# Performance work log

Measured on AMD Instinct MI355X. Metric: run time of the kernel, lower is better.

The kernel has to match this reference:

```python
import jax, jax.numpy as jnp
import numpy as np

N_NODES = 100000
N_EDGES = 600000
N_GRAPHS = 512
VOCAB = 4096
EMB = 128
HID = 128


def setup_inputs() -> dict:
    key = jax.random.key(0)
    ks = jax.random.split(key, 8)
    x = jax.random.randint(ks[0], (N_NODES,), 0, VOCAB)
    edge_index = jax.random.randint(ks[1], (2, N_EDGES), 0, N_NODES)
    batch = jnp.sort(jax.random.randint(ks[2], (N_NODES,), 0, N_GRAPHS))
    emb = jax.random.normal(ks[3], (VOCAB, EMB), dtype=jnp.float32)
    W1 = jax.random.normal(ks[4], (EMB, HID), dtype=jnp.float32) / np.sqrt(EMB)
    b1 = jnp.zeros((HID,), dtype=jnp.float32)
    W2 = jax.random.normal(ks[5], (HID, HID), dtype=jnp.float32) / np.sqrt(HID)
    b2 = jnp.zeros((HID,), dtype=jnp.float32)
    return {"x": x, "edge_index": edge_index, "batch": batch,
            "emb": emb, "W1": W1, "b1": b1, "W2": W2, "b2": b2}


def gcn_conv(h, src, dst, W, b, n_nodes):
    # PyG GCNConv: linear transform, then symmetric-normalized scatter-sum
    # (self-loops already included in src/dst), plus bias.
    h = h @ W
    deg = jax.ops.segment_sum(jnp.ones(dst.shape, h.dtype), dst, num_segments=n_nodes)
    dis = jnp.where(deg > 0, jax.lax.rsqrt(jnp.maximum(deg, 1.0)), 0.0)
    norm = dis[src] * dis[dst]                      # [E]
    msg = h[src] * norm[:, None]                    # gather + scale
    out = jax.ops.segment_sum(msg, dst, num_segments=n_nodes)
    return out + b


def reference(x, edge_index, batch, emb, W1, b1, W2, b2):
    n = x.shape[0]
    loop = jnp.arange(n)
    src = jnp.concatenate([edge_index[0], loop])    # add self-loops, as GCNConv does
    dst = jnp.concatenate([edge_index[1], loop])

    h = emb[x]                                      # [N, EMB] embedding lookup
    h = jax.nn.relu(gcn_conv(h, src, dst, W1, b1, n))
    # dropout: identity in eval mode
    h = gcn_conv(h, src, dst, W2, b2, n)            # [N, HID]

    # global_mean_pool over graph ids
    sums = jax.ops.segment_sum(h, batch, num_segments=N_GRAPHS)
    cnts = jax.ops.segment_sum(jnp.ones((n,), h.dtype), batch, num_segments=N_GRAPHS)
    return sums / jnp.maximum(cnts, 1.0)[:, None]   # [N_GRAPHS, HID]
```

## Files before the change

### kernel.cpp

```cpp
#include <hip/hip_runtime.h>
#include <hip/hip_bf16.h>
#include <hip/hip_fp16.h>

#define D 128

__device__ __forceinline__ float bf2f(unsigned short u) {
  return __uint_as_float(((unsigned int)u) << 16);
}
__device__ __forceinline__ unsigned short f2bf(float f) {
  unsigned int x = __float_as_uint(f);
  x += 0x7fff + ((x >> 16) & 1);
  return (unsigned short)(x >> 16);
}
__device__ __forceinline__ float h2f(unsigned short b) {
  return __half2float(__ushort_as_half(b));
}


__global__ void k_prep(const unsigned short* __restrict__ t0, int n0,
                       const unsigned short* __restrict__ t1, int n1,
                       const unsigned short* __restrict__ t2, int n2,
                       const unsigned short* __restrict__ t3, int n3,
                       const unsigned short* __restrict__ t4, int n4,
                       const unsigned int* __restrict__ ei32,
                       int* __restrict__ flag, int* __restrict__ indeg,
                       float* __restrict__ P, int nn, int ngD) {
  int b = blockIdx.x;
  if (b < 5) {
    const unsigned short* tabs[5] = {t0, t1, t2, t3, t4};
    int ns[5] = {n0, n1, n2, n3, n4};
    const unsigned short* u16 = tabs[b];
    int n = ns[b];
    __shared__ int cnt;
    int K = n / 2 < 256 ? n / 2 : 256;
    if (threadIdx.x == 0) cnt = 0;
    __syncthreads();
    if (threadIdx.x < K) {
      unsigned short u = u16[threadIdx.x * 2];
      int e = (u >> 7) & 0xFF;
      if (u == 0 || (e >= 100 && e <= 140)) atomicAdd(&cnt, 1);
    }
    __syncthreads();
    if (threadIdx.x == 0) flag[b] = (cnt * 2 >= K) ? 1 : 0;
  } else if (b == 5) {
    __shared__ int z;
    if (threadIdx.x == 0) z = 0;
    __syncthreads();
    if (threadIdx.x < 64 && ei32[threadIdx.x * 2 + 1] == 0u) atomicAdd(&z, 1);
    __syncthreads();
    if (threadIdx.x == 0) flag[5] = (z >= 60) ? 1 : 0;
  } else {
    int i = (b - 6) * 256 + threadIdx.x;
    if (i < nn) indeg[i] = 0;
    int j = i - nn;
    if (j >= 0 && j < ngD) P[j] = 0.f;
  }
}

__global__ void k_convi_all(const void* __restrict__ xr, const void* __restrict__ eir,
                            const void* __restrict__ br,
                            int* __restrict__ xs, int* __restrict__ srcs,
                            int* __restrict__ dsts, int* __restrict__ batchs,
                            int* __restrict__ indeg,
                            int nn, int ne, int vocab, int ng,
                            const int* __restrict__ flag64) {
  long long i = (long long)blockIdx.x * blockDim.x + threadIdx.x;
  int is64 = *flag64;
  if (i < nn) {
    int v = is64 ? (int)((const long long*)xr)[i] : ((const int*)xr)[i];
    v = v < 0 ? 0 : (v > vocab - 1 ? vocab - 1 : v);
    xs[i] = v;
  } else if (i < (long long)nn + ne) {
    long long j = i - nn;
    int v = is64 ? (int)((const long long*)eir)[j] : ((const int*)eir)[j];
    v = v < 0 ? 0 : (v > nn - 1 ? nn - 1 : v);
    srcs[j] = v;
  } else if (i < (long long)nn + 2 * ne) {
    long long j = i - nn - ne;
    int v = is64 ? (int)((const long long*)eir)[ne + j] : ((const int*)eir)[ne + j];
    v = v < 0 ? 0 : (v > nn - 1 ? nn - 1 : v);
    dsts[j] = v;
    atomicAdd(&indeg[v], 1);
  } else if (i < 2LL * nn + 2 * ne) {
    long long j = i - nn - 2 * ne;
    int v = is64 ? (int)((const long long*)br)[j] : ((const int*)br)[j];
    v = v < 0 ? 0 : (v > ng - 1 ? ng - 1 : v);
    batchs[j] = v;
  }
}

__global__ __launch_bounds__(1024) void k_scan1(const int* __restrict__ indeg,
                                                int* __restrict__ off,
                                                int* __restrict__ bsum, int nn) {
  int t = threadIdx.x;
  int idx = blockIdx.x * 1024 + t;
  int v = (idx < nn) ? indeg[idx] : 0;
  int lane = t & 63, wid = t >> 6;
  int inc = v;
  #pragma unroll
  for (int d = 1; d < 64; d <<= 1) {
    int u = __shfl_up(inc, d);
    if (lane >= d) inc += u;
  }
  __shared__ int ws[16];
  if (lane == 63) ws[wid] = inc;
  __syncthreads();
  if (wid == 0) {
    int wv = (lane < 16) ? ws[lane] : 0;
    #pragma unroll
    for (int d = 1; d < 16; d <<= 1) {
      int u = __shfl_up(wv, d);
      if (lane >= d) wv += u;
    }
    if (lane < 16) ws[lane] = wv;
  }
  __syncthreads();
  int base = wid ? ws[wid - 1] : 0;
  if (idx < nn) off[idx] = base + inc - v;
  if (t == 1023) bsum[blockIdx.x] = ws[15];
}

__global__ __launch_bounds__(1024) void k_scan23(int* __restrict__ off,
                                                 int* __restrict__ cursor,
                                                 float* __restrict__ dis,
                                                 const int* __restrict__ indeg,
                                                 const int* __restrict__ bsum,
                                                 int nn) {
  int b = blockIdx.x, t = threadIdx.x;
  int v = (t < b) ? bsum[t] : 0;
  #pragma unroll
  for (int d = 32; d; d >>= 1) v += __shfl_xor(v, d);
  __shared__ int ws[16];
  __shared__ int prefix;
  int lane = t & 63, wid = t >> 6;
  if (lane == 0) ws[wid] = v;
  __syncthreads();
  if (t == 0) {
    int s = 0;
    #pragma unroll
    for (int i = 0; i < 16; ++i) s += ws[i];
    prefix = s;
  }
  __syncthreads();
  int idx = b * 1024 + t;
  if (idx < nn) {
    int o = off[idx] + prefix;
    off[idx] = o;
    cursor[idx] = o;
    dis[idx] = rsqrtf((float)indeg[idx] + 1.0f);
  }
}

__global__ void k_fill(const int* __restrict__ srcA, const int* __restrict__ dstA,
                       const int* __restrict__ xs, const float* __restrict__ dis,
                       int* __restrict__ cursor, int2* __restrict__ csr, int ne) {
  int e = blockIdx.x * blockDim.x + threadIdx.x;
  if (e >= ne) return;
  int d = dstA[e], s = srcA[e];
  unsigned short hb = __half_as_ushort(__float2half_rn(dis[s]));
  unsigned int packed = (unsigned int)xs[s] | ((unsigned int)hb << 16);
  int pp = atomicAdd(&cursor[d], 1);
  csr[pp] = make_int2(s, (int)packed);
}

__global__ void k_gemm(const void* __restrict__ emb, const void* __restrict__ W1,
                       float* __restrict__ G, int vocab,
                       const int* __restrict__ flag) {
  int idx = blockIdx.x * blockDim.x + threadIdx.x;
  if (idx >= vocab * D) return;
  int r = idx >> 7, c = idx & 127;
  int fe = flag[0], fw = flag[1];
  const float* ef = (const float*)emb;
  const unsigned short* eu = (const unsigned short*)emb;
  const float* wf = (const float*)W1;
  const unsigned short* wu = (const unsigned short*)W1;
  size_t ro = (size_t)r * D;
  float acc = 0.f;
  if (fe) {
    if (fw) { for (int k = 0; k < D; ++k) acc += bf2f(eu[ro + k]) * bf2f(wu[k * D + c]); }
    else    { for (int k = 0; k < D; ++k) acc += bf2f(eu[ro + k]) * wf[k * D + c]; }
  } else {
    if (fw) { for (int k = 0; k < D; ++k) acc += ef[ro + k] * bf2f(wu[k * D + c]); }
    else    { for (int k = 0; k < D; ++k) acc += ef[ro + k] * wf[k * D + c]; }
  }
  G[idx] = acc;
}

__global__ __launch_bounds__(256) void k_aggrelu(const int* __restrict__ x,
                                                 const float* __restrict__ G,
                                                 const void* __restrict__ b1,
                                                 const int* __restrict__ off,
                                                 const int* __restrict__ indeg,
                                                 const float* __restrict__ dis,
                                                 const int2* __restrict__ csr,
                                                 unsigned short* __restrict__ H1,
                                                 int nn, const int* __restrict__ flag) {
  int gid = blockIdx.x * blockDim.x + threadIdx.x;
  int n = gid >> 6;
  if (n >= nn) return;
  int lane = threadIdx.x & 63;
  float dn = dis[n];
  const float2* G2 = (const float2*)G;
  float2 g0 = G2[(size_t)x[n] * 64 + lane];
  float ax = dn * g0.x, ay = dn * g0.y;
  int s0 = off[n], m = indeg[n];
  int j = 0;
  for (; j + 4 <= m; j += 4) {
    unsigned c0 = (unsigned)csr[s0 + j].y, c1 = (unsigned)csr[s0 + j + 1].y;
    unsigned c2 = (unsigned)csr[s0 + j + 2].y, c3 = (unsigned)csr[s0 + j + 3].y;
    float w0 = h2f((unsigned short)(c0 >> 16));
    float w1 = h2f((unsigned short)(c1 >> 16));
    float w2 = h2f((unsigned short)(c2 >> 16));
    float w3 = h2f((unsigned short)(c3 >> 16));
    float2 gA = G2[(size_t)(c0 & 0xFFFFu) * 64 + lane];
    float2 gB = G2[(size_t)(c1 & 0xFFFFu) * 64 + lane];
    float2 gC = G2[(size_t)(c2 & 0xFFFFu) * 64 + lane];
    float2 gD = G2[(size_t)(c3 & 0xFFFFu) * 64 + lane];
    ax += w0 * gA.x + w1 * gB.x + w2 * gC.x + w3 * gD.x;
    ay += w0 * gA.y + w1 * gB.y + w2 * gC.y + w3 * gD.y;
  }
  for (; j < m; ++j) {
    unsigned c = (unsigned)csr[s0 + j].y;
    float w = h2f((unsigned short)(c >> 16));
    float2 g = G2[(size_t)(c & 0xFFFFu) * 64 + lane];
    ax += w * g.x;
    ay += w * g.y;
  }
  float bx, by;
  if (flag[2]) {
    const unsigned short* bu = (const unsigned short*)b1;
    bx = bf2f(bu[2 * lane]); by = bf2f(bu[2 * lane + 1]);
  } else {
    float2 bb = ((const float2*)b1)[lane];
    bx = bb.x; by = bb.y;
  }
  ushort2 o;
  o.x = f2bf(dn * fmaxf(dn * ax + bx, 0.f));
  o.y = f2bf(dn * fmaxf(dn * ay + by, 0.f));
  ((ushort2*)(H1 + (size_t)n * D))[lane] = o;
}

__global__ __launch_bounds__(512) void k_agg2pool(
    const unsigned short* __restrict__ H1, const int* __restrict__ off,
    const int* __restrict__ indeg, const float* __restrict__ dis,
    const int2* __restrict__ csr, const int* __restrict__ batch,
    float* __restrict__ P, int nn) {
  __shared__ float buf[8][D];
  __shared__ int gbuf[8];
  int t = threadIdx.x;
  int slot = t >> 6, lane = t & 63;
  int n = blockIdx.x * 8 + slot;
  float ax = 0.f, ay = 0.f;
  if (n < nn) {
    float dn = dis[n];
    const ushort2* H2 = (const ushort2*)H1;
    ushort2 u0 = H2[(size_t)n * 64 + lane];
    ax = bf2f(u0.x); ay = bf2f(u0.y);
    int s0 = off[n], m = indeg[n];
    int j = 0;
    for (; j + 4 <= m; j += 4) {
      int e0 = csr[s0 + j].x, e1 = csr[s0 + j + 1].x;
      int e2 = csr[s0 + j + 2].x, e3 = csr[s0 + j + 3].x;
      ushort2 hA = H2[(size_t)e0 * 64 + lane];
      ushort2 hB = H2[(size_t)e1 * 64 + lane];
      ushort2 hC = H2[(size_t)e2 * 64 + lane];
      ushort2 hD = H2[(size_t)e3 * 64 + lane];
      ax += bf2f(hA.x) + bf2f(hB.x) + bf2f(hC.x) + bf2f(hD.x);
      ay += bf2f(hA.y) + bf2f(hB.y) + bf2f(hC.y) + bf2f(hD.y);
    }
    for (; j < m; ++j) {
      int e = csr[s0 + j].x;
      ushort2 h = H2[(size_t)e * 64 + lane];
      ax += bf2f(h.x); ay += bf2f(h.y);
    }
    ax *= dn; ay *= dn;
  }
  ((float2*)&buf[slot][2 * lane])[0] = make_float2(ax, ay);
  if (lane == 0) gbuf[slot] = (n < nn) ? batch[n] : -1;
  __syncthreads();
  if (t < D) {
    int c = t;
    float acc = 0.f;
    int run = -1;
    #pragma unroll
    for (int s2 = 0; s2 < 8; ++s2) {
      int g = gbuf[s2];
      if (g < 0) break;
      if (g != run) {
        if (run >= 0) atomicAdd(&P[(size_t)run * D + c], acc);
        run = g;
        acc = 0.f;
      }
      acc += buf[s2][c];
    }
    if (run >= 0) atomicAdd(&P[(size_t)run * D + c], acc);
  }
}

__global__ void k_out(const float* __restrict__ P, const int* __restrict__ batch,
                      const void* __restrict__ W2, const void* __restrict__ b2,
                      float* __restrict__ Out, int ng, int nn,
                      const int* __restrict__ flag) {
  int idx = blockIdx.x * blockDim.x + threadIdx.x;
  if (idx >= ng * D) return;
  int g = idx >> 7, c = idx & 127;
  int lo = 0, hi = nn;
  while (lo < hi) { int mid = (lo + hi) >> 1; if (batch[mid] < g) lo = mid + 1; else hi = mid; }
  int s = lo;
  hi = nn;
  while (lo < hi) { int mid = (lo + hi) >> 1; if (batch[mid] < g + 1) lo = mid + 1; else hi = mid; }
  int m = lo - s;
  float inv = (m > 0) ? (1.0f / (float)m) : 0.0f;
  const float* pr = P + (size_t)g * D;
  float acc = 0.f;
  if (flag[3]) {
    const unsigned short* wu = (const unsigned short*)W2;
    for (int k = 0; k < D; ++k) acc += pr[k] * bf2f(wu[k * D + c]);
  } else {
    const float* wf = (const float*)W2;
    for (int k = 0; k < D; ++k) acc += pr[k] * wf[k * D + c];
  }
  acc *= inv;
  if (m > 0) acc += flag[4] ? bf2f(((const unsigned short*)b2)[c]) : ((const float*)b2)[c];
  Out[idx] = acc;
}

extern "C" void kernel_launch(void* const* d_in, const int* in_sizes, int n_in,
                              void* d_out, int out_size, void* d_ws, size_t ws_size,
                              hipStream_t stream) {
  const void* xr = d_in[0];
  const void* eir = d_in[1];
  const void* batchr = d_in[2];
  const void* emb = d_in[3];
  const void* W1 = d_in[4];
  const void* b1 = d_in[5];
  const void* W2 = d_in[6];
  const void* b2 = d_in[7];
  float* out = (float*)d_out;

  const int nn = in_sizes[0];
  const int ne = in_sizes[1] / 2;
  const int vocab = in_sizes[3] / D;
  const int ng = out_size / D;
  const int nb = (nn + 1023) / 1024;
  const int ngD = ng * D;

  char* p = (char*)d_ws;
  auto alloc = [&](size_t bytes) -> char* {
    char* r = p;
    p += (bytes + 511) & ~(size_t)511;
    return r;
  };
  int* flag = (int*)alloc(512);
  int* xs = (int*)alloc((size_t)nn * 4);
  int* srcs = (int*)alloc((size_t)ne * 4);
  int* dsts = (int*)alloc((size_t)ne * 4);
  int* batchs = (int*)alloc((size_t)nn * 4);
  int* indeg = (int*)alloc((size_t)nn * 4);
  int* off = (int*)alloc((size_t)nn * 4);
  int* cursor = (int*)alloc((size_t)nn * 4);
  float* dis = (float*)alloc((size_t)nn * 4);
  int* bsum = (int*)alloc((size_t)nb * 4);
  int2* csr = (int2*)alloc((size_t)ne * 8);
  float* G = (float*)alloc((size_t)vocab * D * 4);
  unsigned short* H1 = (unsigned short*)alloc((size_t)nn * D * 2);
  float* P = (float*)alloc((size_t)ngD * 4);

  {
    int zb = (nn + ngD + 255) / 256;
    k_prep<<<6 + zb, 256, 0, stream>>>(
        (const unsigned short*)emb, vocab * D,
        (const unsigned short*)W1, D * D,
        (const unsigned short*)b1, D,
        (const unsigned short*)W2, D * D,
        (const unsigned short*)b2, D,
        (const unsigned int*)eir, flag, indeg, P, nn, ngD);
  }

  {
    long long tot = 2LL * nn + 2LL * ne;
    k_convi_all<<<(int)((tot + 255) / 256), 256, 0, stream>>>(
        xr, eir, batchr, xs, srcs, dsts, batchs, indeg, nn, ne, vocab, ng, flag + 5);
  }

  k_scan1<<<nb, 1024, 0, stream>>>(indeg, off, bsum, nn);
  k_scan23<<<nb, 1024, 0, stream>>>(off, cursor, dis, indeg, bsum, nn);
  k_fill<<<(ne + 255) / 256, 256, 0, stream>>>(srcs, dsts, xs, dis, cursor, csr, ne);

  k_gemm<<<(vocab * D + 255) / 256, 256, 0, stream>>>(emb, W1, G, vocab, flag);

  {
    long long thr = (long long)nn * 64;
    k_aggrelu<<<(int)((thr + 255) / 256), 256, 0, stream>>>(xs, G, b1, off, indeg,
                                                            dis, csr, H1, nn, flag);
  }

  k_agg2pool<<<(nn + 7) / 8, 512, 0, stream>>>(H1, off, indeg, dis, csr,
                                               batchs, P, nn);

  k_out<<<(ngD + 255) / 256, 256, 0, stream>>>(P, batchs, W2, b2, out, ng, nn, flag);
}
```

Baseline: 263.2 us.

## Widen per-lane gathers and software-prefetch CSR indices in both aggregation kernels

The layer-1 aggregation now uses 32 lanes per node, each loading a float4 instead of a float2. The layer-2 aggregate-and-pool kernel uses 16 lanes per node, each loading a 16-byte uint4 of eight bf16 values, and packs 16 nodes per 256-thread block. Both loops software-pipeline the CSR neighbor index loads one iteration ahead. The aim is fewer, wider memory transactions, more nodes per wave and hidden index-load latency, at the cost of more registers per thread and more complex tail handling.

```diff
diff --git a/kernel.cpp b/kernel.cpp
--- a/kernel.cpp
+++ b/kernel.cpp
@@ -14,6 +14,16 @@
 }
 __device__ __forceinline__ float h2f(unsigned short b) {
   return __half2float(__ushort_as_half(b));
+}
+__device__ __forceinline__ void add8(float* a, uint4 v) {
+  a[0] += __uint_as_float(v.x << 16);
+  a[1] += __uint_as_float(v.x & 0xffff0000u);
+  a[2] += __uint_as_float(v.y << 16);
+  a[3] += __uint_as_float(v.y & 0xffff0000u);
+  a[4] += __uint_as_float(v.z << 16);
+  a[5] += __uint_as_float(v.z & 0xffff0000u);
+  a[6] += __uint_as_float(v.w << 16);
+  a[7] += __uint_as_float(v.w & 0xffff0000u);
 }
 
 
@@ -196,86 +206,114 @@
                                                  unsigned short* __restrict__ H1,
                                                  int nn, const int* __restrict__ flag) {
   int gid = blockIdx.x * blockDim.x + threadIdx.x;
-  int n = gid >> 6;
+  int n = gid >> 5;
   if (n >= nn) return;
-  int lane = threadIdx.x & 63;
+  int lane = threadIdx.x & 31;
   float dn = dis[n];
-  const float2* G2 = (const float2*)G;
-  float2 g0 = G2[(size_t)x[n] * 64 + lane];
-  float ax = dn * g0.x, ay = dn * g0.y;
+  float4 g0 = ((const float4*)(G + (size_t)x[n] * D))[lane];
+  float ax = dn * g0.x, ay = dn * g0.y, az = dn * g0.z, aw = dn * g0.w;
   int s0 = off[n], m = indeg[n];
-  int j = 0;
-  for (; j + 4 <= m; j += 4) {
-    unsigned c0 = (unsigned)csr[s0 + j].y, c1 = (unsigned)csr[s0 + j + 1].y;
-    unsigned c2 = (unsigned)csr[s0 + j + 2].y, c3 = (unsigned)csr[s0 + j + 3].y;
-    float w0 = h2f((unsigned short)(c0 >> 16));
-    float w1 = h2f((unsigned short)(c1 >> 16));
-    float w2 = h2f((unsigned short)(c2 >> 16));
-    float w3 = h2f((unsigned short)(c3 >> 16));
-    float2 gA = G2[(size_t)(c0 & 0xFFFFu) * 64 + lane];
-    float2 gB = G2[(size_t)(c1 & 0xFFFFu) * 64 + lane];
-    float2 gC = G2[(size_t)(c2 & 0xFFFFu) * 64 + lane];
-    float2 gD = G2[(size_t)(c3 & 0xFFFFu) * 64 + lane];
-    ax += w0 * gA.x + w1 * gB.x + w2 * gC.x + w3 * gD.x;
-    ay += w0 * gA.y + w1 * gB.y + w2 * gC.y + w3 * gD.y;
-  }
-  for (; j < m; ++j) {
-    unsigned c = (unsigned)csr[s0 + j].y;
-    float w = h2f((unsigned short)(c >> 16));
-    float2 g = G2[(size_t)(c & 0xFFFFu) * 64 + lane];
-    ax += w * g.x;
-    ay += w * g.y;
-  }
-  float bx, by;
+  if (m >= 2) {
+    unsigned int c0 = (unsigned int)csr[s0].y, c1 = (unsigned int)csr[s0 + 1].y;
+    int j = 0;
+    for (; j + 3 < m; j += 2) {
+      unsigned int p0 = (unsigned int)csr[s0 + j + 2].y;
+      unsigned int p1 = (unsigned int)csr[s0 + j + 3].y;
+      float w0 = h2f((unsigned short)(c0 >> 16));
+      float w1 = h2f((unsigned short)(c1 >> 16));
+      float4 gA = ((const float4*)(G + (size_t)(c0 & 0xFFFF) * D))[lane];
+      float4 gB = ((const float4*)(G + (size_t)(c1 & 0xFFFF) * D))[lane];
+      ax += w0 * gA.x + w1 * gB.x;
+      ay += w0 * gA.y + w1 * gB.y;
+      az += w0 * gA.z + w1 * gB.z;
+      aw += w0 * gA.w + w1 * gB.w;
+      c0 = p0; c1 = p1;
+    }
+    {
+      float w0 = h2f((unsigned short)(c0 >> 16));
+      float w1 = h2f((unsigned short)(c1 >> 16));
+      float4 gA = ((const float4*)(G + (size_t)(c0 & 0xFFFF) * D))[lane];
+      float4 gB = ((const float4*)(G + (size_t)(c1 & 0xFFFF) * D))[lane];
+      ax += w0 * gA.x + w1 * gB.x;
+      ay += w0 * gA.y + w1 * gB.y;
+      az += w0 * gA.z + w1 * gB.z;
+      aw += w0 * gA.w + w1 * gB.w;
+    }
+    if (j + 2 < m) {
+      unsigned int e0 = (unsigned int)csr[s0 + j + 2].y;
+      float w0 = h2f((unsigned short)(e0 >> 16));
+      float4 gA = ((const float4*)(G + (size_t)(e0 & 0xFFFF) * D))[lane];
+      ax += w0 * gA.x; ay += w0 * gA.y; az += w0 * gA.z; aw += w0 * gA.w;
+    }
+  } else if (m == 1) {
+    unsigned int e0 = (unsigned int)csr[s0].y;
+    float w0 = h2f((unsigned short)(e0 >> 16));
+    float4 gA = ((const float4*)(G + (size_t)(e0 & 0xFFFF) * D))[lane];
+    ax += w0 * gA.x; ay += w0 * gA.y; az += w0 * gA.z; aw += w0 * gA.w;
+  }
+  float4 bb;
   if (flag[2]) {
-    const unsigned short* bu = (const unsigned short*)b1;
-    bx = bf2f(bu[2 * lane]); by = bf2f(bu[2 * lane + 1]);
+    ushort4 bu = ((const ushort4*)b1)[lane];
+    bb = make_float4(bf2f(bu.x), bf2f(bu.y), bf2f(bu.z), bf2f(bu.w));
   } else {
-    float2 bb = ((const float2*)b1)[lane];
-    bx = bb.x; by = bb.y;
-  }
-  ushort2 o;
-  o.x = f2bf(dn * fmaxf(dn * ax + bx, 0.f));
-  o.y = f2bf(dn * fmaxf(dn * ay + by, 0.f));
-  ((ushort2*)(H1 + (size_t)n * D))[lane] = o;
-}
-
-__global__ __launch_bounds__(512) void k_agg2pool(
+    bb = ((const float4*)b1)[lane];
+  }
+  ushort4 o;
+  o.x = f2bf(dn * fmaxf(dn * ax + bb.x, 0.f));
+  o.y = f2bf(dn * fmaxf(dn * ay + bb.y, 0.f));
+  o.z = f2bf(dn * fmaxf(dn * az + bb.z, 0.f));
+  o.w = f2bf(dn * fmaxf(dn * aw + bb.w, 0.f));
+  ((ushort4*)(H1 + (size_t)n * D))[lane] = o;
+}
+
+__global__ __launch_bounds__(256) void k_agg2pool(
     const unsigned short* __restrict__ H1, const int* __restrict__ off,
     const int* __restrict__ indeg, const float* __restrict__ dis,
     const int2* __restrict__ csr, const int* __restrict__ batch,
     float* __restrict__ P, int nn) {
-  __shared__ float buf[8][D];
-  __shared__ int gbuf[8];
+  __shared__ float buf[16][D];
+  __shared__ int gbuf[16];
   int t = threadIdx.x;
-  int slot = t >> 6, lane = t & 63;
-  int n = blockIdx.x * 8 + slot;
-  float ax = 0.f, ay = 0.f;
+  int slot = t >> 4, lane = t & 15;
+  int n = blockIdx.x * 16 + slot;
+  float a[8] = {0.f, 0.f, 0.f, 0.f, 0.f, 0.f, 0.f, 0.f};
   if (n < nn) {
     float dn = dis[n];
-    const ushort2* H2 = (const ushort2*)H1;
-    ushort2 u0 = H2[(size_t)n * 64 + lane];
-    ax = bf2f(u0.x); ay = bf2f(u0.y);
+    const uint4* H4 = (const uint4*)H1;
+    add8(a, H4[(size_t)n * 16 + lane]);
     int s0 = off[n], m = indeg[n];
     int j = 0;
-    for (; j + 4 <= m; j += 4) {
-      int e0 = csr[s0 + j].x, e1 = csr[s0 + j + 1].x;
-      int e2 = csr[s0 + j + 2].x, e3 = csr[s0 + j + 3].x;
-      ushort2 hA = H2[(size_t)e0 * 64 + lane];
-      ushort2 hB = H2[(size_t)e1 * 64 + lane];
-      ushort2 hC = H2[(size_t)e2 * 64 + lane];
-      ushort2 hD = H2[(size_t)e3 * 64 + lane];
-      ax += bf2f(hA.x) + bf2f(hB.x) + bf2f(hC.x) + bf2f(hD.x);
-      ay += bf2f(hA.y) + bf2f(hB.y) + bf2f(hC.y) + bf2f(hD.y);
+    if (m >= 4) {
+      int i0 = csr[s0].x, i1 = csr[s0 + 1].x;
+      int i2 = csr[s0 + 2].x, i3 = csr[s0 + 3].x;
+      for (; j + 8 <= m; j += 4) {
+        int p0 = csr[s0 + j + 4].x, p1 = csr[s0 + j + 5].x;
+        int p2 = csr[s0 + j + 6].x, p3 = csr[s0 + j + 7].x;
+        uint4 vA = H4[(size_t)i0 * 16 + lane];
+        uint4 vB = H4[(size_t)i1 * 16 + lane];
+        uint4 vC = H4[(size_t)i2 * 16 + lane];
+        uint4 vD = H4[(size_t)i3 * 16 + lane];
+        add8(a, vA); add8(a, vB); add8(a, vC); add8(a, vD);
+        i0 = p0; i1 = p1; i2 = p2; i3 = p3;
+      }
+      {
+        uint4 vA = H4[(size_t)i0 * 16 + lane];
+        uint4 vB = H4[(size_t)i1 * 16 + lane];
+        uint4 vC = H4[(size_t)i2 * 16 + lane];
+        uint4 vD = H4[(size_t)i3 * 16 + lane];
+        add8(a, vA); add8(a, vB); add8(a, vC); add8(a, vD);
+      }
+      j += 4;
     }
     for (; j < m; ++j) {
       int e = csr[s0 + j].x;
-      ushort2 h = H2[(size_t)e * 64 + lane];
-      ax += bf2f(h.x); ay += bf2f(h.y);
-    }
-    ax *= dn; ay *= dn;
-  }
-  ((float2*)&buf[slot][2 * lane])[0] = make_float2(ax, ay);
+      add8(a, H4[(size_t)e * 16 + lane]);
+    }
+    #pragma unroll
+    for (int q = 0; q < 8; ++q) a[q] *= dn;
+  }
+  ((float4*)&buf[slot][lane * 8])[0] = make_float4(a[0], a[1], a[2], a[3]);
+  ((float4*)&buf[slot][lane * 8])[1] = make_float4(a[4], a[5], a[6], a[7]);
   if (lane == 0) gbuf[slot] = (n < nn) ? batch[n] : -1;
   __syncthreads();
   if (t < D) {
@@ -283,7 +321,7 @@
     float acc = 0.f;
     int run = -1;
     #pragma unroll
-    for (int s2 = 0; s2 < 8; ++s2) {
+    for (int s2 = 0; s2 < 16; ++s2) {
       int g = gbuf[s2];
       if (g < 0) break;
       if (g != run) {
@@ -390,13 +428,13 @@
   k_gemm<<<(vocab * D + 255) / 256, 256, 0, stream>>>(emb, W1, G, vocab, flag);
 
   {
-    long long thr = (long long)nn * 64;
+    long long thr = (long long)nn * 32;
     k_aggrelu<<<(int)((thr + 255) / 256), 256, 0, stream>>>(xs, G, b1, off, indeg,
                                                             dis, csr, H1, nn, flag);
   }
 
-  k_agg2pool<<<(nn + 7) / 8, 512, 0, stream>>>(H1, off, indeg, dis, csr,
-                                               batchs, P, nn);
+  k_agg2pool<<<(nn + 15) / 16, 256, 0, stream>>>(H1, off, indeg, dis, csr,
+                                                 batchs, P, nn);
 
   k_out<<<(ngD + 255) / 256, 256, 0, stream>>>(P, batchs, W2, b2, out, ng, nn, flag);
 }
```

New measurement: 223.7 us. 15.0% less time.
